# Optimization experiments

Measured on AMD Instinct MI355X. Metric: run time of the kernel, lower is better.

## Reference

```python
import jax, jax.numpy as jnp
import numpy as np

N, E, G = 50000, 400000, 2000
H, HEADS, HD = 128, 4, 32


def setup_inputs() -> dict:
    key = jax.random.key(0)
    ks = jax.random.split(key, 16)
    nrm = lambda k, shape, s=0.05: jax.random.normal(k, shape, dtype=jnp.float32) * s
    inp = {}
    inp["x"] = jax.random.normal(ks[0], (N, 39), dtype=jnp.float32)
    inp["edge_index"] = jax.random.randint(ks[1], (2, E), 0, N, dtype=jnp.int32)
    inp["edge_attr"] = jax.random.normal(ks[2], (E, 8), dtype=jnp.float32)
    inp["batch"] = jnp.sort(jax.random.randint(ks[3], (N,), 0, G, dtype=jnp.int32))
    inp["in_W"] = nrm(ks[4], (39, H)); inp["in_b"] = jnp.zeros((H,), jnp.float32)
    inp["in_g"] = jnp.ones((H,), jnp.float32); inp["in_beta"] = jnp.zeros((H,), jnp.float32)
    inp["Wl"] = nrm(ks[5], (3, H, H)); inp["Wr"] = nrm(ks[6], (3, H, H))
    inp["We"] = nrm(ks[7], (3, 8, H)); inp["att"] = nrm(ks[8], (3, HEADS, HD))
    inp["conv_b"] = jnp.zeros((3, H), jnp.float32)
    inp["bn_g"] = jnp.ones((3, H), jnp.float32); inp["bn_b"] = jnp.zeros((3, H), jnp.float32)
    inp["t1_W"] = nrm(ks[9], (3 * H, 256)); inp["t1_b"] = jnp.zeros((256,), jnp.float32)
    inp["t1_g"] = jnp.ones((256,), jnp.float32); inp["t1_beta"] = jnp.zeros((256,), jnp.float32)
    inp["t2_W"] = nrm(ks[10], (256, 128)); inp["t2_b"] = jnp.zeros((128,), jnp.float32)
    inp["t2_g"] = jnp.ones((128,), jnp.float32); inp["t2_beta"] = jnp.zeros((128,), jnp.float32)
    inp["head_W"] = nrm(ks[11], (128, 12)); inp["head_b"] = jnp.zeros((12,), jnp.float32)
    return inp


def _bn(h, g, b):
    # BatchNorm1d in training mode: normalize with batch statistics.
    m = h.mean(0)
    v = ((h - m) ** 2).mean(0)
    return g * (h - m) * jax.lax.rsqrt(v + 1e-5) + b


def reference(x, edge_index, edge_attr, batch, in_W, in_b, in_g, in_beta,
              Wl, Wr, We, att, conv_b, bn_g, bn_b,
              t1_W, t1_b, t1_g, t1_beta, t2_W, t2_b, t2_g, t2_beta,
              head_W, head_b):
    src, dst = edge_index[0], edge_index[1]  # messages flow src -> dst (PyG convention)
    xn = jax.nn.relu(_bn(x @ in_W + in_b, in_g, in_beta))  # [N, H]
    for l in range(3):  # three residual GATv2 layers
        xl = (xn @ Wl[l]).reshape(N, HEADS, HD)  # lin_l (source transform)
        xr = (xn @ Wr[l]).reshape(N, HEADS, HD)  # lin_r (target transform)
        ep = (edge_attr @ We[l]).reshape(E, HEADS, HD)
        m = jax.nn.leaky_relu(xl[src] + xr[dst] + ep, 0.2)  # [E, HEADS, HD]
        alpha = jnp.einsum('ehd,hd->eh', m, att[l])  # [E, HEADS]
        amax = jax.ops.segment_max(alpha, dst, num_segments=N)
        amax = jnp.where(jnp.isfinite(amax), amax, 0.0)  # nodes with no in-edges
        ae = jnp.exp(alpha - amax[dst])
        denom = jax.ops.segment_sum(ae, dst, num_segments=N)
        a = ae / (denom[dst] + 1e-16)  # scatter-softmax over neighborhoods
        agg = jax.ops.segment_sum(xl[src] * a[:, :, None], dst, num_segments=N)
        h = agg.reshape(N, H) + conv_b[l]
        h = jax.nn.elu(_bn(h, bn_g[l], bn_b[l]))
        xn = xn + h
    # 3-way global pooling per graph
    cnt = jax.ops.segment_sum(jnp.ones((N,), jnp.float32), batch, num_segments=G)
    sadd = jax.ops.segment_sum(xn, batch, num_segments=G)
    smean = sadd / jnp.maximum(cnt, 1.0)[:, None]
    smax = jax.ops.segment_max(xn, batch, num_segments=G)
    smax = jnp.where(cnt[:, None] > 0, smax, 0.0)
    xg = jnp.concatenate([smean, smax, sadd], axis=1)  # [G, 3H]
    t = jax.nn.relu(_bn(xg @ t1_W + t1_b, t1_g, t1_beta))
    t = jax.nn.relu(_bn(t @ t2_W + t2_b, t2_g, t2_beta))
    return jax.nn.sigmoid(t @ head_W + head_b)  # [G, 12]
```

## Files before the change

kernel.cpp:

```cpp
#include <hip/hip_runtime.h>
#include <math.h>


constexpr int N_ = 50000;
constexpr int E_ = 400000;
constexpr int G_ = 2000;
constexpr int H_ = 128;
constexpr int IN_ = 39;

typedef __attribute__((ext_vector_type(8))) short bf16x8;
typedef __attribute__((ext_vector_type(4))) float f32x4;

__device__ __forceinline__ unsigned pk_bf16(float a, float b) {
  unsigned ua = __float_as_uint(a);
  unsigned ub = __float_as_uint(b);
  ua = (ua + 0x7fffu + ((ua >> 16) & 1u)) >> 16;
  ub = (ub + 0x7fffu + ((ub >> 16) & 1u)) & 0xffff0000u;
  return ua | ub;
}
__device__ __forceinline__ unsigned short bf16_1(float x) {
  unsigned u = __float_as_uint(x);
  u = (u + 0x7fffu + ((u >> 16) & 1u)) >> 16;
  return (unsigned short)u;
}
__device__ __forceinline__ float up_lo(unsigned u) { return __uint_as_float(u << 16); }
__device__ __forceinline__ float up_hi(unsigned u) { return __uint_as_float(u & 0xffff0000u); }

__global__ __launch_bounds__(256) void hist_kernel(const int* __restrict__ keys, int n,
                                                   int* __restrict__ cnt) {
  for (int i = blockIdx.x * 256 + threadIdx.x; i < n; i += gridDim.x * 256)
    atomicAdd(&cnt[keys[i]], 1);
}

__global__ __launch_bounds__(1024) void scan_local(const int* __restrict__ in,
                                                   int* __restrict__ outx,
                                                   int* __restrict__ bsum, int n) {
  __shared__ int wsum[16];
  int t = threadIdx.x, lane = t & 63, wid = t >> 6;
  int idx = blockIdx.x * 1024 + t;
  int v = (idx < n) ? in[idx] : 0;
  int x = v;
#pragma unroll
  for (int off = 1; off < 64; off <<= 1) {
    int y = __shfl_up(x, off, 64);
    if (lane >= off) x += y;
  }
  if (lane == 63) wsum[wid] = x;
  __syncthreads();
  if (t == 0) {
    int acc = 0;
#pragma unroll
    for (int w = 0; w < 16; w++) { int tmp = wsum[w]; wsum[w] = acc; acc += tmp; }
    bsum[blockIdx.x] = acc;
  }
  __syncthreads();
  if (idx < n) outx[idx] = wsum[wid] + x - v;
}

__global__ __launch_bounds__(64) void scan_bsum(const int* __restrict__ bsum,
                                                int* __restrict__ boff, int nb) {
  int t = threadIdx.x;
  int v = (t < nb) ? bsum[t] : 0;
  int x = v;
#pragma unroll
  for (int off = 1; off < 64; off <<= 1) {
    int y = __shfl_up(x, off, 64);
    if (t >= off) x += y;
  }
  boff[t] = x - v;
}

__global__ __launch_bounds__(1024) void scan_add(int* __restrict__ eoff,
                                                 const int* __restrict__ boff,
                                                 int* __restrict__ cursor, int n) {
  int idx = blockIdx.x * 1024 + threadIdx.x;
  if (idx < n) {
    int e = eoff[idx] + boff[idx >> 10];
    eoff[idx] = e;
    cursor[idx] = e;
  }
  if (idx == 0) eoff[n] = E_;
}

__global__ __launch_bounds__(256) void goff_from_sorted(const int* __restrict__ batch,
                                                        int* __restrict__ goff) {
  int i = blockIdx.x * 256 + threadIdx.x;
  if (i >= N_) return;
  int bi = batch[i];
  int bp = (i == 0) ? -1 : batch[i - 1];
  for (int g = bp + 1; g <= bi; g++) goff[g] = i;
  if (i == N_ - 1) {
    for (int g = bi + 1; g <= G_; g++) goff[g] = N_;
  }
}

__global__ __launch_bounds__(256) void edge_scatter(const int* __restrict__ ei,
                                                    const float* __restrict__ ea,
                                                    int* __restrict__ cursor,
                                                    int* __restrict__ esrc,
                                                    unsigned* __restrict__ easb) {
  int e = blockIdx.x * 256 + threadIdx.x;
  if (e >= E_) return;
  int src = ei[e];
  int dst = ei[E_ + e];
  int j = atomicAdd(&cursor[dst], 1);
  esrc[j] = src;
  const float4* eav = (const float4*)(ea + (size_t)e * 8);
  float4 a0 = eav[0], a1 = eav[1];
  uint4 o;
  o.x = pk_bf16(a0.x, a0.y);
  o.y = pk_bf16(a0.z, a0.w);
  o.z = pk_bf16(a1.x, a1.y);
  o.w = pk_bf16(a1.z, a1.w);
  ((uint4*)easb)[j] = o;
}

__global__ __launch_bounds__(256) void pack_weights(const float* __restrict__ Wl,
                                                    const float* __restrict__ Wr,
                                                    unsigned short* __restrict__ wpack) {
  int i = blockIdx.x * 256 + threadIdx.x;
  if (i >= 3 * 128 * 256) return;
  int l = i >> 15;
  int rem = i & 32767;
  int k = rem >> 8;
  int n = rem & 255;
  const float* Wsrc = (n < 128) ? (Wl + l * H_ * H_) : (Wr + l * H_ * H_);
  int nn = n & 127;
  wpack[(size_t)l * 32768 + n * 128 + k] = bf16_1(Wsrc[k * H_ + nn]);
}

__global__ __launch_bounds__(256) void in_gemm(const float* __restrict__ x,
                                               const float* __restrict__ W,
                                               const float* __restrict__ b,
                                               float* __restrict__ y,
                                               float* __restrict__ ssum,
                                               float* __restrict__ ssq) {
  __shared__ float xs[32][40];
  __shared__ float s1[256], s2[256];
  int t = threadIdx.x;
  int row0 = blockIdx.x * 32;
  for (int i = t; i < 32 * IN_; i += 256) {
    int r = i / IN_, k = i % IN_;
    int row = row0 + r;
    xs[r][k] = (row < N_) ? x[row * IN_ + k] : 0.f;
  }
  __syncthreads();
  int col = t & 127;
  int half = t >> 7;
  float acc[16];
#pragma unroll
  for (int r = 0; r < 16; r++) acc[r] = 0.f;
  for (int k = 0; k < IN_; k++) {
    float w = W[k * H_ + col];
#pragma unroll
    for (int r = 0; r < 16; r++) acc[r] = fmaf(xs[half * 16 + r][k], w, acc[r]);
  }
  float bb = b[col];
  float a1 = 0.f, a2 = 0.f;
#pragma unroll
  for (int r = 0; r < 16; r++) {
    int row = row0 + half * 16 + r;
    float v = acc[r] + bb;
    if (row < N_) {
      y[row * H_ + col] = v;
      a1 += v;
      a2 = fmaf(v, v, a2);
    }
  }
  s1[t] = a1; s2[t] = a2;
  __syncthreads();
  if (t < 128) {
    atomicAdd(&ssum[t], s1[t] + s1[t + 128]);
    atomicAdd(&ssq[t], s2[t] + s2[t + 128]);
  }
}

template <int MODE>
__global__ __launch_bounds__(256) void gemm_mfma(float* __restrict__ xn,
                                                 const float* __restrict__ buf,
                                                 const float* __restrict__ g,
                                                 const float* __restrict__ beta,
                                                 const float* __restrict__ ssum,
                                                 const float* __restrict__ ssq,
                                                 float rows_inv,
                                                 const unsigned short* __restrict__ wp,
                                                 unsigned* __restrict__ xlb,
                                                 unsigned* __restrict__ xrb) {
  __shared__ short a_s[64][136];
  __shared__ short b_s[256][40];
  int t = threadIdx.x;
  int lane = t & 63, w = t >> 6;
  int quad = lane >> 4, lc = lane & 15;
  int row0 = blockIdx.x * 64;

  {
    int r = t >> 2;
    int row = row0 + r;
    int kb0 = (t & 3) * 32;
    bool valid = row < N_;
    for (int kk = 0; kk < 32; kk += 4) {
      int c = kb0 + kk;
      float4 v = make_float4(0.f, 0.f, 0.f, 0.f);
      if (valid) {
        float4 bv = *(const float4*)&buf[(size_t)row * H_ + c];
        float4 gv = *(const float4*)&g[c];
        float4 be = *(const float4*)&beta[c];
        float4 s1 = *(const float4*)&ssum[c];
        float4 s2 = *(const float4*)&ssq[c];
        float m0 = s1.x * rows_inv, m1 = s1.y * rows_inv;
        float m2 = s1.z * rows_inv, m3 = s1.w * rows_inv;
        float r0 = rsqrtf(s2.x * rows_inv - m0 * m0 + 1e-5f);
        float r1 = rsqrtf(s2.y * rows_inv - m1 * m1 + 1e-5f);
        float r2 = rsqrtf(s2.z * rows_inv - m2 * m2 + 1e-5f);
        float r3 = rsqrtf(s2.w * rows_inv - m3 * m3 + 1e-5f);
        float t0 = gv.x * (bv.x - m0) * r0 + be.x;
        float t1 = gv.y * (bv.y - m1) * r1 + be.y;
        float t2 = gv.z * (bv.z - m2) * r2 + be.z;
        float t3 = gv.w * (bv.w - m3) * r3 + be.w;
        if (MODE == 1) {
          v = make_float4(fmaxf(t0, 0.f), fmaxf(t1, 0.f), fmaxf(t2, 0.f), fmaxf(t3, 0.f));
        } else {
          float4 xo = *(const float4*)&xn[(size_t)row * H_ + c];
          v.x = xo.x + ((t0 > 0.f) ? t0 : (__expf(t0) - 1.f));
          v.y = xo.y + ((t1 > 0.f) ? t1 : (__expf(t1) - 1.f));
          v.z = xo.z + ((t2 > 0.f) ? t2 : (__expf(t2) - 1.f));
          v.w = xo.w + ((t3 > 0.f) ? t3 : (__expf(t3) - 1.f));
        }
        *(float4*)&xn[(size_t)row * H_ + c] = v;
      }
      uint2 pk;
      pk.x = pk_bf16(v.x, v.y);
      pk.y = pk_bf16(v.z, v.w);
      *(uint2*)&a_s[r][c] = pk;
    }
  }

  f32x4 acc[16];
#pragma unroll
  for (int nt = 0; nt < 16; nt++) acc[nt] = (f32x4){0.f, 0.f, 0.f, 0.f};

  for (int kb = 0; kb < 4; kb++) {
    __syncthreads();
    for (int i = t; i < 1024; i += 256) {
      int n = i >> 2;
      int k8 = (i & 3) * 8;
      *(uint4*)&b_s[n][k8] = *(const uint4*)&wp[(size_t)n * 128 + kb * 32 + k8];
    }
    __syncthreads();
    bf16x8 av = *(const bf16x8*)&a_s[w * 16 + lc][kb * 32 + quad * 8];
#pragma unroll
    for (int nt = 0; nt < 16; nt++) {
      bf16x8 bv = *(const bf16x8*)&b_s[nt * 16 + lc][quad * 8];
      acc[nt] = __builtin_amdgcn_mfma_f32_16x16x32_bf16(av, bv, acc[nt], 0, 0, 0);
    }
  }

  int rowg0 = row0 + w * 16 + quad * 4;
#pragma unroll
  for (int nt = 0; nt < 16; nt++) {
    unsigned* xout = (nt < 8) ? xlb : xrb;
    int cp0 = (nt & 7) * 8;
#pragma unroll
    for (int rr = 0; rr < 4; rr++) {
      float v = acc[nt][rr];
      float pv = __shfl_xor(v, 1, 64);
      int rowg = rowg0 + rr;
      if (!(lc & 1) && rowg < N_) {
        unsigned u = pk_bf16(v, pv);
        xout[(size_t)rowg * 64 + cp0 + (lc >> 1)] = u;
      }
    }
  }
}

__device__ __forceinline__ float ep8u(const uint4& u, const float* w) {
  float ep = up_lo(u.x) * w[0];
  ep = fmaf(up_hi(u.x), w[1], ep);
  ep = fmaf(up_lo(u.y), w[2], ep);
  ep = fmaf(up_hi(u.y), w[3], ep);
  ep = fmaf(up_lo(u.z), w[4], ep);
  ep = fmaf(up_hi(u.z), w[5], ep);
  ep = fmaf(up_lo(u.w), w[6], ep);
  ep = fmaf(up_hi(u.w), w[7], ep);
  return ep;
}

__global__ __launch_bounds__(256) void agg_csr(const int* __restrict__ eoff,
                                               const int* __restrict__ esrc,
                                               const unsigned* __restrict__ easb,
                                               const float* __restrict__ Wel,
                                               const float* __restrict__ attl,
                                               const unsigned* __restrict__ xlb,
                                               const unsigned* __restrict__ xrb,
                                               const float* __restrict__ cb,
                                               float* __restrict__ buf,
                                               float* __restrict__ ssum,
                                               float* __restrict__ ssq) {
  __shared__ float sA[256], sB[256], sC[256], sD[256];
  int t = threadIdx.x;
  int l = t & 63;
  int sub = t >> 6;
  int c0 = l * 2;
  float w0[8], w1[8];
#pragma unroll
  for (int k = 0; k < 8; k++) {
    float2 wv = *(const float2*)&Wel[k * H_ + c0];
    w0[k] = wv.x; w1[k] = wv.y;
  }
  float2 attv = *(const float2*)&attl[c0];
  float2 cbv = *(const float2*)&cb[c0];
  const uint4* eas4 = (const uint4*)easb;
  float a1_0 = 0.f, a1_1 = 0.f, a2_0 = 0.f, a2_1 = 0.f;
  for (int n = blockIdx.x * 4 + sub; n < N_; n += gridDim.x * 4) {
    unsigned xru = xrb[(size_t)n * 64 + l];
    float xr0 = up_lo(xru), xr1 = up_hi(xru);
    int e0 = eoff[n], e1 = eoff[n + 1];
    float acc0 = 0.f, acc1 = 0.f, den = 0.f;
    int j = e0;
    for (; j + 4 <= e1; j += 4) {
      int s0 = esrc[j], s1 = esrc[j + 1], s2 = esrc[j + 2], s3 = esrc[j + 3];
      uint4 u0 = eas4[j], u1 = eas4[j + 1], u2 = eas4[j + 2], u3 = eas4[j + 3];
      unsigned xu0 = xlb[(size_t)s0 * 64 + l];
      unsigned xu1 = xlb[(size_t)s1 * 64 + l];
      unsigned xu2 = xlb[(size_t)s2 * 64 + l];
      unsigned xu3 = xlb[(size_t)s3 * 64 + l];
      float x00 = up_lo(xu0), x01 = up_hi(xu0);
      float x10 = up_lo(xu1), x11 = up_hi(xu1);
      float x20 = up_lo(xu2), x21 = up_hi(xu2);
      float x30 = up_lo(xu3), x31 = up_hi(xu3);
      float m00 = x00 + xr0 + ep8u(u0, w0);
      float m01 = x01 + xr1 + ep8u(u0, w1);
      float m10 = x10 + xr0 + ep8u(u1, w0);
      float m11 = x11 + xr1 + ep8u(u1, w1);
      float m20 = x20 + xr0 + ep8u(u2, w0);
      float m21 = x21 + xr1 + ep8u(u2, w1);
      float m30 = x30 + xr0 + ep8u(u3, w0);
      float m31 = x31 + xr1 + ep8u(u3, w1);
      m00 = (m00 > 0.f) ? m00 : 0.2f * m00;
      m01 = (m01 > 0.f) ? m01 : 0.2f * m01;
      m10 = (m10 > 0.f) ? m10 : 0.2f * m10;
      m11 = (m11 > 0.f) ? m11 : 0.2f * m11;
      m20 = (m20 > 0.f) ? m20 : 0.2f * m20;
      m21 = (m21 > 0.f) ? m21 : 0.2f * m21;
      m30 = (m30 > 0.f) ? m30 : 0.2f * m30;
      m31 = (m31 > 0.f) ? m31 : 0.2f * m31;
      float p0 = fmaf(m00, attv.x, m01 * attv.y);
      float p1 = fmaf(m10, attv.x, m11 * attv.y);
      float p2 = fmaf(m20, attv.x, m21 * attv.y);
      float p3 = fmaf(m30, attv.x, m31 * attv.y);
#pragma unroll
      for (int off = 8; off > 0; off >>= 1) {
        p0 += __shfl_xor(p0, off, 64);
        p1 += __shfl_xor(p1, off, 64);
        p2 += __shfl_xor(p2, off, 64);
        p3 += __shfl_xor(p3, off, 64);
      }
      float e0v = __expf(p0), e1v = __expf(p1), e2v = __expf(p2), e3v = __expf(p3);
      acc0 = fmaf(e0v, x00, acc0); acc1 = fmaf(e0v, x01, acc1);
      acc0 = fmaf(e1v, x10, acc0); acc1 = fmaf(e1v, x11, acc1);
      acc0 = fmaf(e2v, x20, acc0); acc1 = fmaf(e2v, x21, acc1);
      acc0 = fmaf(e3v, x30, acc0); acc1 = fmaf(e3v, x31, acc1);
      den += (e0v + e1v) + (e2v + e3v);
    }
    for (; j < e1; j++) {
      int s0 = esrc[j];
      uint4 u0 = eas4[j];
      unsigned xu0 = xlb[(size_t)s0 * 64 + l];
      float x00 = up_lo(xu0), x01 = up_hi(xu0);
      float m00 = x00 + xr0 + ep8u(u0, w0);
      float m01 = x01 + xr1 + ep8u(u0, w1);
      m00 = (m00 > 0.f) ? m00 : 0.2f * m00;
      m01 = (m01 > 0.f) ? m01 : 0.2f * m01;
      float p0 = fmaf(m00, attv.x, m01 * attv.y);
#pragma unroll
      for (int off = 8; off > 0; off >>= 1) p0 += __shfl_xor(p0, off, 64);
      float e0v = __expf(p0);
      acc0 = fmaf(e0v, x00, acc0);
      acc1 = fmaf(e0v, x01, acc1);
      den += e0v;
    }
    float inv = 1.f / (den + 1e-16f);
    float h0 = acc0 * inv + cbv.x;
    float h1 = acc1 * inv + cbv.y;
    *(float2*)&buf[(size_t)n * H_ + c0] = make_float2(h0, h1);
    a1_0 += h0; a1_1 += h1;
    a2_0 = fmaf(h0, h0, a2_0); a2_1 = fmaf(h1, h1, a2_1);
  }
  sA[t] = a1_0; sB[t] = a1_1; sC[t] = a2_0; sD[t] = a2_1;
  __syncthreads();
  if (t < 64) {
    float r1 = sA[t] + sA[t + 64] + sA[t + 128] + sA[t + 192];
    float r2 = sB[t] + sB[t + 64] + sB[t + 128] + sB[t + 192];
    float r3 = sC[t] + sC[t + 64] + sC[t + 128] + sC[t + 192];
    float r4 = sD[t] + sD[t + 64] + sD[t + 128] + sD[t + 192];
    atomicAdd(&ssum[2 * t], r1);
    atomicAdd(&ssum[2 * t + 1], r2);
    atomicAdd(&ssq[2 * t], r3);
    atomicAdd(&ssq[2 * t + 1], r4);
  }
}

__global__ __launch_bounds__(256) void apply_bn_relu(const float* __restrict__ y,
                                                     float* __restrict__ out,
                                                     const float* __restrict__ g,
                                                     const float* __restrict__ beta,
                                                     const float* __restrict__ ssum,
                                                     const float* __restrict__ ssq,
                                                     float rows_inv,
                                                     long total, int cmask) {
  long i = (long)blockIdx.x * 256 + threadIdx.x;
  if (i >= total) return;
  int c = (int)i & cmask;
  float m = ssum[c] * rows_inv;
  float rs = rsqrtf(ssq[c] * rows_inv - m * m + 1e-5f);
  float v = g[c] * (y[i] - m) * rs + beta[c];
  out[i] = fmaxf(v, 0.f);
}

__global__ __launch_bounds__(128) void pool_residual(const int* __restrict__ goff,
                                                     const float* __restrict__ xn,
                                                     const float* __restrict__ buf,
                                                     const float* __restrict__ g,
                                                     const float* __restrict__ beta,
                                                     const float* __restrict__ ssum,
                                                     const float* __restrict__ ssq,
                                                     float rows_inv,
                                                     float* __restrict__ xg) {
  int gr = blockIdx.x;
  int t = threadIdx.x;
  int n0 = goff[gr], n1 = goff[gr + 1];
  float mm = ssum[t] * rows_inv;
  float rr = rsqrtf(ssq[t] * rows_inv - mm * mm + 1e-5f);
  float gg = g[t], bb = beta[t];
  float s = 0.f, mx = -INFINITY;
  for (int n = n0; n < n1; n++) {
    float w = gg * (buf[(size_t)n * H_ + t] - mm) * rr + bb;
    w = (w > 0.f) ? w : (__expf(w) - 1.f);
    float v = xn[(size_t)n * H_ + t] + w;
    s += v;
    mx = fmaxf(mx, v);
  }
  float c = (float)(n1 - n0);
  xg[gr * 384 + t] = s / fmaxf(c, 1.f);
  xg[gr * 384 + 128 + t] = (c > 0.f) ? mx : 0.f;
  xg[gr * 384 + 256 + t] = s;
}

template <int K, int COLS>
__global__ void mlp_gemm(const float* __restrict__ A, const float* __restrict__ W,
                         const float* __restrict__ b, float* __restrict__ Y, int rows,
                         float* __restrict__ ssum, float* __restrict__ ssq) {
  __shared__ float xs[8][K];
  int t = threadIdx.x;
  int row0 = blockIdx.x * 8;
  for (int i = t; i < 8 * K; i += COLS) {
    int r = i / K, k = i % K;
    int row = row0 + r;
    xs[r][k] = (row < rows) ? A[row * K + k] : 0.f;
  }
  __syncthreads();
  float acc[8];
#pragma unroll
  for (int r = 0; r < 8; r++) acc[r] = 0.f;
  for (int k = 0; k < K; k++) {
    float w = W[k * COLS + t];
#pragma unroll
    for (int r = 0; r < 8; r++) acc[r] = fmaf(xs[r][k], w, acc[r]);
  }
  float bb = b[t];
  float a1 = 0.f, a2 = 0.f;
#pragma unroll
  for (int r = 0; r < 8; r++) {
    int row = row0 + r;
    if (row < rows) {
      float v = acc[r] + bb;
      Y[row * COLS + t] = v;
      a1 += v;
      a2 = fmaf(v, v, a2);
    }
  }
  atomicAdd(&ssum[t], a1);
  atomicAdd(&ssq[t], a2);
}

__global__ __launch_bounds__(64) void head_kernel(const float* __restrict__ u,
                                                  const float* __restrict__ W,
                                                  const float* __restrict__ b,
                                                  float* __restrict__ out) {
  __shared__ float row[128];
  int g = blockIdx.x;
  int t = threadIdx.x;
  row[t] = u[g * 128 + t];
  row[t + 64] = u[g * 128 + 64 + t];
  __syncthreads();
  if (t < 12) {
    float acc = b[t];
    for (int k = 0; k < 128; k++) acc = fmaf(row[k], W[k * 12 + t], acc);
    out[g * 12 + t] = 1.f / (1.f + expf(-acc));
  }
}

extern "C" void kernel_launch(void* const* d_in, const int* in_sizes, int n_in, void* d_out,
                              int out_size, void* d_ws, size_t ws_size, hipStream_t stream) {
  (void)in_sizes; (void)n_in; (void)out_size; (void)ws_size;
  const float* x       = (const float*)d_in[0];
  const int*   ei      = (const int*)d_in[1];
  const float* ea      = (const float*)d_in[2];
  const int*   batch   = (const int*)d_in[3];
  const float* in_W    = (const float*)d_in[4];
  const float* in_b    = (const float*)d_in[5];
  const float* in_g    = (const float*)d_in[6];
  const float* in_beta = (const float*)d_in[7];
  const float* Wl      = (const float*)d_in[8];
  const float* Wr      = (const float*)d_in[9];
  const float* We      = (const float*)d_in[10];
  const float* att     = (const float*)d_in[11];
  const float* conv_b  = (const float*)d_in[12];
  const float* bn_g    = (const float*)d_in[13];
  const float* bn_b    = (const float*)d_in[14];
  const float* t1_W    = (const float*)d_in[15];
  const float* t1_b    = (const float*)d_in[16];
  const float* t1_g    = (const float*)d_in[17];
  const float* t1_beta = (const float*)d_in[18];
  const float* t2_W    = (const float*)d_in[19];
  const float* t2_b    = (const float*)d_in[20];
  const float* t2_g    = (const float*)d_in[21];
  const float* t2_beta = (const float*)d_in[22];
  const float* head_W  = (const float*)d_in[23];
  const float* head_b  = (const float*)d_in[24];
  float* out = (float*)d_out;

  float* p = (float*)d_ws;
  float* xn    = p; p += N_ * H_;
  float* buf   = p; p += N_ * H_;
  float* sstat = p; p += 6 * 512;
  float* xg    = p; p += G_ * 384;
  float* u1    = p; p += G_ * 256;
  float* u2    = p; p += G_ * 128;
  unsigned* up = (unsigned*)p;
  unsigned* xlb  = up; up += (size_t)N_ * 64;
  unsigned* xrb  = up; up += (size_t)N_ * 64;
  unsigned* easb = up; up += (size_t)E_ * 4;
  unsigned short* wpack = (unsigned short*)up; up += 3 * 32768 / 2;
  int* ip = (int*)up;
  int* deg    = ip; ip += N_;
  int* eoff   = ip; ip += N_ + 1;
  int* cursor = ip; ip += N_;
  int* goff   = ip; ip += G_ + 1;
  int* esrc   = ip; ip += E_;
  int* bsum   = ip; ip += 64;
  int* boff   = ip; ip += 64;

#define SSUM(s) (sstat + (s) * 512)
#define SSQ(s)  (sstat + (s) * 512 + 256)

  hipMemsetAsync(deg, 0, (size_t)N_ * sizeof(int), stream);
  hipMemsetAsync(sstat, 0, 6 * 512 * sizeof(float), stream);
  hist_kernel<<<1024, 256, 0, stream>>>(ei + E_, E_, deg);
  scan_local<<<49, 1024, 0, stream>>>(deg, eoff, bsum, N_);
  scan_bsum<<<1, 64, 0, stream>>>(bsum, boff, 49);
  scan_add<<<49, 1024, 0, stream>>>(eoff, boff, cursor, N_);
  edge_scatter<<<(E_ + 255) / 256, 256, 0, stream>>>(ei, ea, cursor, esrc, easb);
  goff_from_sorted<<<(N_ + 255) / 256, 256, 0, stream>>>(batch, goff);
  pack_weights<<<384, 256, 0, stream>>>(Wl, Wr, wpack);

  in_gemm<<<(N_ + 31) / 32, 256, 0, stream>>>(x, in_W, in_b, buf, SSUM(0), SSQ(0));

  const float rnInv = 1.f / N_;
  const int GT = (N_ + 63) / 64;
  gemm_mfma<1><<<GT, 256, 0, stream>>>(xn, buf, in_g, in_beta, SSUM(0), SSQ(0), rnInv,
                                       wpack, xlb, xrb);
  agg_csr<<<2048, 256, 0, stream>>>(eoff, esrc, easb, We, att, xlb, xrb, conv_b,
                                    buf, SSUM(1), SSQ(1));
  gemm_mfma<2><<<GT, 256, 0, stream>>>(xn, buf, bn_g, bn_b, SSUM(1), SSQ(1), rnInv,
                                       wpack + 32768, xlb, xrb);
  agg_csr<<<2048, 256, 0, stream>>>(eoff, esrc, easb, We + 8 * H_, att + H_, xlb, xrb,
                                    conv_b + H_, buf, SSUM(2), SSQ(2));
  gemm_mfma<2><<<GT, 256, 0, stream>>>(xn, buf, bn_g + H_, bn_b + H_, SSUM(2), SSQ(2),
                                       rnInv, wpack + 65536, xlb, xrb);
  agg_csr<<<2048, 256, 0, stream>>>(eoff, esrc, easb, We + 16 * H_, att + 2 * H_, xlb, xrb,
                                    conv_b + 2 * H_, buf, SSUM(3), SSQ(3));

  pool_residual<<<G_, 128, 0, stream>>>(goff, xn, buf, bn_g + 2 * H_, bn_b + 2 * H_,
                                        SSUM(3), SSQ(3), rnInv, xg);

  const float rgInv = 1.f / G_;
  mlp_gemm<384, 256><<<G_ / 8, 256, 0, stream>>>(xg, t1_W, t1_b, u1, G_, SSUM(4), SSQ(4));
  apply_bn_relu<<<(G_ * 256 + 255) / 256, 256, 0, stream>>>(u1, u1, t1_g, t1_beta,
                                                            SSUM(4), SSQ(4), rgInv,
                                                            (long)G_ * 256, 255);

  mlp_gemm<256, 128><<<G_ / 8, 128, 0, stream>>>(u1, t2_W, t2_b, u2, G_, SSUM(5), SSQ(5));
  apply_bn_relu<<<(G_ * 128 + 255) / 256, 256, 0, stream>>>(u2, u2, t2_g, t2_beta,
                                                            SSUM(5), SSQ(5), rgInv,
                                                            (long)G_ * 128, 127);

  head_kernel<<<G_, 64, 0, stream>>>(u2, head_W, head_b, out);
#undef SSUM
#undef SSQ
}
```

Baseline: 866.8 us.

## Merge setup kernels, fold BN+ReLU into MLP consumers, double agg grid

```diff
diff --git a/kernel.cpp b/kernel.cpp
--- a/kernel.cpp
+++ b/kernel.cpp
@@ -57,76 +57,81 @@
   if (idx < n) outx[idx] = wsum[wid] + x - v;
 }
 
-__global__ __launch_bounds__(64) void scan_bsum(const int* __restrict__ bsum,
-                                                int* __restrict__ boff, int nb) {
-  int t = threadIdx.x;
-  int v = (t < nb) ? bsum[t] : 0;
-  int x = v;
-#pragma unroll
-  for (int off = 1; off < 64; off <<= 1) {
-    int y = __shfl_up(x, off, 64);
-    if (t >= off) x += y;
-  }
-  boff[t] = x - v;
-}
-
 __global__ __launch_bounds__(1024) void scan_add(int* __restrict__ eoff,
-                                                 const int* __restrict__ boff,
+                                                 const int* __restrict__ bsum,
                                                  int* __restrict__ cursor, int n) {
-  int idx = blockIdx.x * 1024 + threadIdx.x;
+  __shared__ int boff_s;
+  int t = threadIdx.x;
+  if (t < 64) {
+    int v = (t < 49) ? bsum[t] : 0;
+    int x = v;
+#pragma unroll
+    for (int off = 1; off < 64; off <<= 1) {
+      int y = __shfl_up(x, off, 64);
+      if (t >= off) x += y;
+    }
+    if (t == (int)blockIdx.x) boff_s = x - v;
+  }
+  __syncthreads();
+  int idx = blockIdx.x * 1024 + t;
   if (idx < n) {
-    int e = eoff[idx] + boff[idx >> 10];
+    int e = eoff[idx] + boff_s;
     eoff[idx] = e;
     cursor[idx] = e;
   }
   if (idx == 0) eoff[n] = E_;
 }
 
-__global__ __launch_bounds__(256) void goff_from_sorted(const int* __restrict__ batch,
-                                                        int* __restrict__ goff) {
-  int i = blockIdx.x * 256 + threadIdx.x;
-  if (i >= N_) return;
-  int bi = batch[i];
-  int bp = (i == 0) ? -1 : batch[i - 1];
-  for (int g = bp + 1; g <= bi; g++) goff[g] = i;
-  if (i == N_ - 1) {
-    for (int g = bi + 1; g <= G_; g++) goff[g] = N_;
-  }
-}
-
-__global__ __launch_bounds__(256) void edge_scatter(const int* __restrict__ ei,
-                                                    const float* __restrict__ ea,
-                                                    int* __restrict__ cursor,
-                                                    int* __restrict__ esrc,
-                                                    unsigned* __restrict__ easb) {
-  int e = blockIdx.x * 256 + threadIdx.x;
-  if (e >= E_) return;
-  int src = ei[e];
-  int dst = ei[E_ + e];
-  int j = atomicAdd(&cursor[dst], 1);
-  esrc[j] = src;
-  const float4* eav = (const float4*)(ea + (size_t)e * 8);
-  float4 a0 = eav[0], a1 = eav[1];
-  uint4 o;
-  o.x = pk_bf16(a0.x, a0.y);
-  o.y = pk_bf16(a0.z, a0.w);
-  o.z = pk_bf16(a1.x, a1.y);
-  o.w = pk_bf16(a1.z, a1.w);
-  ((uint4*)easb)[j] = o;
-}
-
-__global__ __launch_bounds__(256) void pack_weights(const float* __restrict__ Wl,
-                                                    const float* __restrict__ Wr,
-                                                    unsigned short* __restrict__ wpack) {
-  int i = blockIdx.x * 256 + threadIdx.x;
-  if (i >= 3 * 128 * 256) return;
-  int l = i >> 15;
-  int rem = i & 32767;
-  int k = rem >> 8;
-  int n = rem & 255;
-  const float* Wsrc = (n < 128) ? (Wl + l * H_ * H_) : (Wr + l * H_ * H_);
-  int nn = n & 127;
-  wpack[(size_t)l * 32768 + n * 128 + k] = bf16_1(Wsrc[k * H_ + nn]);
+__global__ __launch_bounds__(256) void build_misc(const int* __restrict__ ei,
+                                                  const float* __restrict__ ea,
+                                                  int* __restrict__ cursor,
+                                                  int* __restrict__ esrc,
+                                                  unsigned* __restrict__ easb,
+                                                  const int* __restrict__ batch,
+                                                  int* __restrict__ goff,
+                                                  const float* __restrict__ Wl,
+                                                  const float* __restrict__ Wr,
+                                                  unsigned short* __restrict__ wpack,
+                                                  float* __restrict__ sstat) {
+  int b = blockIdx.x;
+  int t = threadIdx.x;
+  if (b < 1563) {
+    int e = b * 256 + t;
+    if (e >= E_) return;
+    int src = ei[e];
+    int dst = ei[E_ + e];
+    int j = atomicAdd(&cursor[dst], 1);
+    esrc[j] = src;
+    const float4* eav = (const float4*)(ea + (size_t)e * 8);
+    float4 a0 = eav[0], a1 = eav[1];
+    uint4 o;
+    o.x = pk_bf16(a0.x, a0.y);
+    o.y = pk_bf16(a0.z, a0.w);
+    o.z = pk_bf16(a1.x, a1.y);
+    o.w = pk_bf16(a1.z, a1.w);
+    ((uint4*)easb)[j] = o;
+  } else if (b < 1759) {
+    int i = (b - 1563) * 256 + t;
+    if (i >= N_) return;
+    int bi = batch[i];
+    int bp = (i == 0) ? -1 : batch[i - 1];
+    for (int g = bp + 1; g <= bi; g++) goff[g] = i;
+    if (i == N_ - 1) {
+      for (int g = bi + 1; g <= G_; g++) goff[g] = N_;
+    }
+  } else if (b < 2143) {
+    int i = (b - 1759) * 256 + t;
+    if (i >= 3 * 128 * 256) return;
+    int l = i >> 15;
+    int rem = i & 32767;
+    int k = rem >> 8;
+    int n = rem & 255;
+    const float* Wsrc = (n < 128) ? (Wl + l * H_ * H_) : (Wr + l * H_ * H_);
+    int nn = n & 127;
+    wpack[(size_t)l * 32768 + n * 128 + k] = bf16_1(Wsrc[k * H_ + nn]);
+  } else {
+    for (int i = t; i < 6 * 512; i += 256) sstat[i] = 0.f;
+  }
 }
 
 __global__ __launch_bounds__(256) void in_gemm(const float* __restrict__ x,
@@ -400,23 +405,6 @@
   }
 }
 
-__global__ __launch_bounds__(256) void apply_bn_relu(const float* __restrict__ y,
-                                                     float* __restrict__ out,
-                                                     const float* __restrict__ g,
-                                                     const float* __restrict__ beta,
-                                                     const float* __restrict__ ssum,
-                                                     const float* __restrict__ ssq,
-                                                     float rows_inv,
-                                                     long total, int cmask) {
-  long i = (long)blockIdx.x * 256 + threadIdx.x;
-  if (i >= total) return;
-  int c = (int)i & cmask;
-  float m = ssum[c] * rows_inv;
-  float rs = rsqrtf(ssq[c] * rows_inv - m * m + 1e-5f);
-  float v = g[c] * (y[i] - m) * rs + beta[c];
-  out[i] = fmaxf(v, 0.f);
-}
-
 __global__ __launch_bounds__(128) void pool_residual(const int* __restrict__ goff,
                                                      const float* __restrict__ xn,
                                                      const float* __restrict__ buf,
@@ -446,24 +434,25 @@
   xg[gr * 384 + 256 + t] = s;
 }
 
-template <int K, int COLS>
-__global__ void mlp_gemm(const float* __restrict__ A, const float* __restrict__ W,
-                         const float* __restrict__ b, float* __restrict__ Y, int rows,
-                         float* __restrict__ ssum, float* __restrict__ ssq) {
-  __shared__ float xs[8][K];
+__global__ __launch_bounds__(256) void mlp_gemm_t1(const float* __restrict__ A,
+                                                   const float* __restrict__ W,
+                                                   const float* __restrict__ b,
+                                                   float* __restrict__ Y,
+                                                   float* __restrict__ ssum,
+                                                   float* __restrict__ ssq) {
+  __shared__ float xs[8][384];
   int t = threadIdx.x;
   int row0 = blockIdx.x * 8;
-  for (int i = t; i < 8 * K; i += COLS) {
-    int r = i / K, k = i % K;
-    int row = row0 + r;
-    xs[r][k] = (row < rows) ? A[row * K + k] : 0.f;
+  for (int i = t; i < 8 * 384; i += 256) {
+    int r = i / 384, k = i % 384;
+    xs[r][k] = A[(row0 + r) * 384 + k];
   }
   __syncthreads();
   float acc[8];
 #pragma unroll
   for (int r = 0; r < 8; r++) acc[r] = 0.f;
-  for (int k = 0; k < K; k++) {
-    float w = W[k * COLS + t];
+  for (int k = 0; k < 384; k++) {
+    float w = W[k * 256 + t];
 #pragma unroll
     for (int r = 0; r < 8; r++) acc[r] = fmaf(xs[r][k], w, acc[r]);
   }
@@ -471,32 +460,83 @@
   float a1 = 0.f, a2 = 0.f;
 #pragma unroll
   for (int r = 0; r < 8; r++) {
-    int row = row0 + r;
-    if (row < rows) {
-      float v = acc[r] + bb;
-      Y[row * COLS + t] = v;
-      a1 += v;
-      a2 = fmaf(v, v, a2);
-    }
+    float v = acc[r] + bb;
+    Y[(row0 + r) * 256 + t] = v;
+    a1 += v;
+    a2 = fmaf(v, v, a2);
   }
   atomicAdd(&ssum[t], a1);
   atomicAdd(&ssq[t], a2);
 }
 
-__global__ __launch_bounds__(64) void head_kernel(const float* __restrict__ u,
+__global__ __launch_bounds__(128) void mlp_gemm_t2(const float* __restrict__ u1,
+                                                   const float* __restrict__ g1,
+                                                   const float* __restrict__ be1,
+                                                   const float* __restrict__ ssum1,
+                                                   const float* __restrict__ ssq1,
+                                                   float rows_inv,
+                                                   const float* __restrict__ W,
+                                                   const float* __restrict__ b,
+                                                   float* __restrict__ Y,
+                                                   float* __restrict__ ssum,
+                                                   float* __restrict__ ssq) {
+  __shared__ float xs[8][256];
+  int t = threadIdx.x;
+  int row0 = blockIdx.x * 8;
+  for (int i = t; i < 8 * 256; i += 128) {
+    int r = i >> 8, k = i & 255;
+    float raw = u1[(row0 + r) * 256 + k];
+    float m = ssum1[k] * rows_inv;
+    float rs = rsqrtf(ssq1[k] * rows_inv - m * m + 1e-5f);
+    xs[r][k] = fmaxf(g1[k] * (raw - m) * rs + be1[k], 0.f);
+  }
+  __syncthreads();
+  float acc[8];
+#pragma unroll
+  for (int r = 0; r < 8; r++) acc[r] = 0.f;
+  for (int k = 0; k < 256; k++) {
+    float w = W[k * 128 + t];
+#pragma unroll
+    for (int r = 0; r < 8; r++) acc[r] = fmaf(xs[r][k], w, acc[r]);
+  }
+  float bb = b[t];
+  float a1 = 0.f, a2 = 0.f;
+#pragma unroll
+  for (int r = 0; r < 8; r++) {
+    float v = acc[r] + bb;
+    Y[(row0 + r) * 128 + t] = v;
+    a1 += v;
+    a2 = fmaf(v, v, a2);
+  }
+  atomicAdd(&ssum[t], a1);
+  atomicAdd(&ssq[t], a2);
+}
+
+__global__ __launch_bounds__(64) void head_kernel(const float* __restrict__ u2,
+                                                  const float* __restrict__ g2,
+                                                  const float* __restrict__ be2,
+                                                  const float* __restrict__ ssum2,
+                                                  const float* __restrict__ ssq2,
+                                                  float rows_inv,
                                                   const float* __restrict__ W,
                                                   const float* __restrict__ b,
                                                   float* __restrict__ out) {
   __shared__ float row[128];
-  int g = blockIdx.x;
-  int t = threadIdx.x;
-  row[t] = u[g * 128 + t];
-  row[t + 64] = u[g * 128 + 64 + t];
+  int gidx = blockIdx.x;
+  int t = threadIdx.x;
+#pragma unroll
+  for (int h = 0; h < 2; h++) {
+    int k = t + h * 64;
+    float raw = u2[gidx * 128 + k];
+    float m = ssum2[k] * rows_inv;
+    float rs = rsqrtf(ssq2[k] * rows_inv - m * m + 1e-5f);
+    row[k] = fmaxf(g2[k] * (raw - m) * rs + be2[k], 0.f);
+  }
   __syncthreads();
   if (t < 12) {
     float acc = b[t];
     for (int k = 0; k < 128; k++) acc = fmaf(row[k], W[k * 12 + t], acc);
-    out[g * 12 + t] = 1.f / (1.f + expf(-acc));
+    out[gidx * 12 + t] = 1.f / (1.f + expf(-acc));
   }
 }
 
@@ -549,20 +589,16 @@
   int* goff   = ip; ip += G_ + 1;
   int* esrc   = ip; ip += E_;
   int* bsum   = ip; ip += 64;
-  int* boff   = ip; ip += 64;
 
 #define SSUM(s) (sstat + (s) * 512)
 #define SSQ(s)  (sstat + (s) * 512 + 256)
 
   hipMemsetAsync(deg, 0, (size_t)N_ * sizeof(int), stream);
-  hipMemsetAsync(sstat, 0, 6 * 512 * sizeof(float), stream);
   hist_kernel<<<1024, 256, 0, stream>>>(ei + E_, E_, deg);
   scan_local<<<49, 1024, 0, stream>>>(deg, eoff, bsum, N_);
-  scan_bsum<<<1, 64, 0, stream>>>(bsum, boff, 49);
-  scan_add<<<49, 1024, 0, stream>>>(eoff, boff, cursor, N_);
-  edge_scatter<<<(E_ + 255) / 256, 256, 0, stream>>>(ei, ea, cursor, esrc, easb);
-  goff_from_sorted<<<(N_ + 255) / 256, 256, 0, stream>>>(batch, goff);
-  pack_weights<<<384, 256, 0, stream>>>(Wl, Wr, wpack);
+  scan_add<<<49, 1024, 0, stream>>>(eoff, bsum, cursor, N_);
+  build_misc<<<2144, 256, 0, stream>>>(ei, ea, cursor, esrc, easb, batch, goff,
+                                       Wl, Wr, wpack, sstat);
 
   in_gemm<<<(N_ + 31) / 32, 256, 0, stream>>>(x, in_W, in_b, buf, SSUM(0), SSQ(0));
 
@@ -570,32 +606,26 @@
   const int GT = (N_ + 63) / 64;
   gemm_mfma<1><<<GT, 256, 0, stream>>>(xn, buf, in_g, in_beta, SSUM(0), SSQ(0), rnInv,
                                        wpack, xlb, xrb);
-  agg_csr<<<2048, 256, 0, stream>>>(eoff, esrc, easb, We, att, xlb, xrb, conv_b,
+  agg_csr<<<4096, 256, 0, stream>>>(eoff, esrc, easb, We, att, xlb, xrb, conv_b,
                                     buf, SSUM(1), SSQ(1));
   gemm_mfma<2><<<GT, 256, 0, stream>>>(xn, buf, bn_g, bn_b, SSUM(1), SSQ(1), rnInv,
                                        wpack + 32768, xlb, xrb);
-  agg_csr<<<2048, 256, 0, stream>>>(eoff, esrc, easb, We + 8 * H_, att + H_, xlb, xrb,
+  agg_csr<<<4096, 256, 0, stream>>>(eoff, esrc, easb, We + 8 * H_, att + H_, xlb, xrb,
                                     conv_b + H_, buf, SSUM(2), SSQ(2));
   gemm_mfma<2><<<GT, 256, 0, stream>>>(xn, buf, bn_g + H_, bn_b + H_, SSUM(2), SSQ(2),
                                        rnInv, wpack + 65536, xlb, xrb);
-  agg_csr<<<2048, 256, 0, stream>>>(eoff, esrc, easb, We + 16 * H_, att + 2 * H_, xlb, xrb,
+  agg_csr<<<4096, 256, 0, stream>>>(eoff, esrc, easb, We + 16 * H_, att + 2 * H_, xlb, xrb,
                                     conv_b + 2 * H_, buf, SSUM(3), SSQ(3));
 
   pool_residual<<<G_, 128, 0, stream>>>(goff, xn, buf, bn_g + 2 * H_, bn_b + 2 * H_,
                                         SSUM(3), SSQ(3), rnInv, xg);
 
   const float rgInv = 1.f / G_;
-  mlp_gemm<384, 256><<<G_ / 8, 256, 0, stream>>>(xg, t1_W, t1_b, u1, G_, SSUM(4), SSQ(4));
-  apply_bn_relu<<<(G_ * 256 + 255) / 256, 256, 0, stream>>>(u1, u1, t1_g, t1_beta,
-                                                            SSUM(4), SSQ(4), rgInv,
-                                                            (long)G_ * 256, 255);
-
-  mlp_gemm<256, 128><<<G_ / 8, 128, 0, stream>>>(u1, t2_W, t2_b, u2, G_, SSUM(5), SSQ(5));
-  apply_bn_relu<<<(G_ * 128 + 255) / 256, 256, 0, stream>>>(u2, u2, t2_g, t2_beta,
-                                                            SSUM(5), SSQ(5), rgInv,
-                                                            (long)G_ * 128, 127);
-
-  head_kernel<<<G_, 64, 0, stream>>>(u2, head_W, head_b, out);
+  mlp_gemm_t1<<<G_ / 8, 256, 0, stream>>>(xg, t1_W, t1_b, u1, SSUM(4), SSQ(4));
+  mlp_gemm_t2<<<G_ / 8, 128, 0, stream>>>(u1, t1_g, t1_beta, SSUM(4), SSQ(4), rgInv,
+                                          t2_W, t2_b, u2, SSUM(5), SSQ(5));
+  head_kernel<<<G_, 64, 0, stream>>>(u2, t2_g, t2_beta, SSUM(5), SSQ(5), rgInv,
+                                     head_W, head_b, out);
 #undef SSUM
 #undef SSQ
 }
```

After: 1.103 ms. 1.27x slower.
